# Kernel optimization log

Hardware: AMD Instinct MI355X
Metric: run time of the kernel (lower is better)

Reference implementation:

```python
import jax, jax.numpy as jnp
import numpy as np


def setup_inputs() -> dict:
    key = jax.random.key(0)
    ks = jax.random.split(key, 5)
    B, T, I, H = 32, 2048, 512, 512
    scale = 1.0 / np.sqrt(H)
    return {
        "x": jax.random.normal(ks[0], (B, T, I), dtype=jnp.float32),
        "h_0": jnp.zeros((B, H), dtype=jnp.float32),
        "Wx": jax.random.normal(ks[1], (H, I), dtype=jnp.float32) * scale,
        "bx": jax.random.normal(ks[2], (H,), dtype=jnp.float32) * scale,
        "Wh": jax.random.normal(ks[3], (H, H), dtype=jnp.float32) * scale,
        "bh": jax.random.normal(ks[4], (H,), dtype=jnp.float32) * scale,
    }


def reference(x, h_0, Wx, bx, Wh, bh):
    # Precompute input projection for all timesteps in one big GEMM: [B,T,H]
    x_proj = jnp.einsum("bti,hi->bth", x, Wx) + bx + bh

    def step(h, xp_t):  # h: [B,H], xp_t: [B,H]
        h_new = jnp.tanh(xp_t + h @ Wh.T)
        return h_new, h_new

    # scan over time axis: move T to leading dim
    h_last, outs = jax.lax.scan(step, h_0, jnp.swapaxes(x_proj, 0, 1))
    outputs = jnp.swapaxes(outs, 0, 1)  # [B,T,H]
    return outputs, h_last
```

## Files before the change

### kernel.cpp

```cpp
#include <hip/hip_runtime.h>


constexpr int Bb = 32, Tt = 2048, Ii = 512, Hh = 512;
constexpr int NP = 8;
constexpr int RP = Hh / NP;

static __device__ __forceinline__ float fast_tanh(float x) {
    float ax = fabsf(x);
    float e = __expf(-2.0f * ax);
    float r = (1.0f - e) / (1.0f + e);
    return copysignf(r, x);
}

__global__ __launch_bounds__(256, 2)
void xproj_gemm(const float* __restrict__ x, const float* __restrict__ Wx,
                const float* __restrict__ bx, const float* __restrict__ bh,
                float* __restrict__ xp)
{
    constexpr int BM = 128, BK = 16, LDT = BM + 4;
    __shared__ float As[BK][LDT];
    __shared__ float Bs[BK][LDT];

    const int tid = threadIdx.x;
    const int m0 = blockIdx.x * BM;
    const int n0 = blockIdx.y * BM;
    const int lrow = tid >> 1;
    const int lkh  = (tid & 1) * 8;
    const int tx = tid & 15, ty = tid >> 4;

    float acc[2][2][4][4] = {};

    for (int k0 = 0; k0 < Ii; k0 += BK) {
        float4 a0 = *reinterpret_cast<const float4*>(&x[(size_t)(m0 + lrow) * Ii + k0 + lkh]);
        float4 a1 = *reinterpret_cast<const float4*>(&x[(size_t)(m0 + lrow) * Ii + k0 + lkh + 4]);
        float4 b0 = *reinterpret_cast<const float4*>(&Wx[(size_t)(n0 + lrow) * Ii + k0 + lkh]);
        float4 b1 = *reinterpret_cast<const float4*>(&Wx[(size_t)(n0 + lrow) * Ii + k0 + lkh + 4]);
        __syncthreads();
        As[lkh + 0][lrow] = a0.x; As[lkh + 1][lrow] = a0.y;
        As[lkh + 2][lrow] = a0.z; As[lkh + 3][lrow] = a0.w;
        As[lkh + 4][lrow] = a1.x; As[lkh + 5][lrow] = a1.y;
        As[lkh + 6][lrow] = a1.z; As[lkh + 7][lrow] = a1.w;
        Bs[lkh + 0][lrow] = b0.x; Bs[lkh + 1][lrow] = b0.y;
        Bs[lkh + 2][lrow] = b0.z; Bs[lkh + 3][lrow] = b0.w;
        Bs[lkh + 4][lrow] = b1.x; Bs[lkh + 5][lrow] = b1.y;
        Bs[lkh + 6][lrow] = b1.z; Bs[lkh + 7][lrow] = b1.w;
        __syncthreads();
        #pragma unroll
        for (int k = 0; k < BK; ++k) {
            float4 av[2], bv[2];
            av[0] = *reinterpret_cast<const float4*>(&As[k][ty * 4]);
            av[1] = *reinterpret_cast<const float4*>(&As[k][64 + ty * 4]);
            bv[0] = *reinterpret_cast<const float4*>(&Bs[k][tx * 4]);
            bv[1] = *reinterpret_cast<const float4*>(&Bs[k][64 + tx * 4]);
            #pragma unroll
            for (int rh = 0; rh < 2; ++rh) {
                const float* ap = reinterpret_cast<const float*>(&av[rh]);
                #pragma unroll
                for (int ch = 0; ch < 2; ++ch) {
                    const float* bp = reinterpret_cast<const float*>(&bv[ch]);
                    #pragma unroll
                    for (int i = 0; i < 4; ++i)
                        #pragma unroll
                        for (int j = 0; j < 4; ++j)
                            acc[rh][ch][i][j] += ap[i] * bp[j];
                }
            }
        }
    }

    float4 bias[2];
    #pragma unroll
    for (int ch = 0; ch < 2; ++ch) {
        int cb = n0 + ch * 64 + tx * 4;
        bias[ch] = make_float4(bx[cb] + bh[cb], bx[cb + 1] + bh[cb + 1],
                               bx[cb + 2] + bh[cb + 2], bx[cb + 3] + bh[cb + 3]);
    }
    #pragma unroll
    for (int rh = 0; rh < 2; ++rh)
        #pragma unroll
        for (int i = 0; i < 4; ++i) {
            size_t row = (size_t)(m0 + rh * 64 + ty * 4 + i);
            #pragma unroll
            for (int ch = 0; ch < 2; ++ch) {
                const float* bp = reinterpret_cast<const float*>(&bias[ch]);
                float4 v = make_float4(acc[rh][ch][i][0] + bp[0], acc[rh][ch][i][1] + bp[1],
                                       acc[rh][ch][i][2] + bp[2], acc[rh][ch][i][3] + bp[3]);
                *reinterpret_cast<float4*>(&xp[row * Hh + n0 + ch * 64 + tx * 4]) = v;
            }
        }
}

__global__ void zero_xbuf(unsigned long long* __restrict__ xb)
{
    xb[(size_t)blockIdx.x * 512 + threadIdx.x] = 0ull;
}

__global__ __launch_bounds__(512, 1)
void rnn_scan_mb(const float* __restrict__ Wh, const float* __restrict__ h0,
                 float* __restrict__ out, unsigned long long* __restrict__ xbuf)
{
    const int bid = blockIdx.x;
    const int c = bid & 31;
    const int P = bid >> 5;
    const int tid = threadIdx.x;
    const int w = tid >> 6;
    const int lane = tid & 63;
    const int hf = lane >> 5, lp = lane & 31;
    const int lrow0 = w * 8 + hf * 4;

    __shared__ __align__(16) float hs[Hh];
    __shared__ __align__(16) float pacc[RP][36];

    float4 wreg[4][4];
    #pragma unroll
    for (int s = 0; s < 4; ++s)
        #pragma unroll
        for (int q = 0; q < 4; ++q) {
            const float* ap = &Wh[(size_t)(P * RP + lrow0 + s) * Hh + q * 128 + lp * 4];
            asm volatile("global_load_dwordx4 %0, %1, off"
                         : "=v"(wreg[s][q]) : "v"(ap));
        }
    asm volatile("s_waitcnt vmcnt(0)" ::: "memory");

    hs[tid] = h0[(size_t)c * Hh + tid];

    float* ob = out + (size_t)c * Tt * Hh;
    unsigned long long* xb = xbuf + (size_t)c * 2 * Hh;

    float xp_cur = 0.f;
    if (w == P) xp_cur = ob[P * RP + lane];
    __syncthreads();

    for (int t = 0; t < Tt; ++t) {
        float4 hv[4];
        #pragma unroll
        for (int q = 0; q < 4; ++q)
            hv[q] = *reinterpret_cast<const float4*>(&hs[q * 128 + lp * 4]);
        #pragma unroll
        for (int s = 0; s < 4; ++s) {
            float sum = 0.f;
            #pragma unroll
            for (int q = 0; q < 4; ++q) {
                const float* wq = reinterpret_cast<const float*>(&wreg[s][q]);
                const float* hq = reinterpret_cast<const float*>(&hv[q]);
                sum += wq[0] * hq[0]; sum += wq[1] * hq[1];
                sum += wq[2] * hq[2]; sum += wq[3] * hq[3];
            }
            pacc[lrow0 + s][lp] = sum;
        }
        __syncthreads();

        if (w == P) {
            float ssum = xp_cur;
            #pragma unroll
            for (int q = 0; q < 8; ++q) {
                float4 p4 = *reinterpret_cast<const float4*>(&pacc[lane][q * 4]);
                ssum += (p4.x + p4.y) + (p4.z + p4.w);
            }
            float hval = fast_tanh(ssum);
            ob[(size_t)t * Hh + P * RP + lane] = hval;
            if (t + 1 < Tt) {
                unsigned long long msg =
                    ((unsigned long long)(unsigned)(t + 1) << 32) |
                    (unsigned long long)__float_as_uint(hval);
                __hip_atomic_store(&xb[(size_t)(t & 1) * Hh + P * RP + lane], msg,
                                   __ATOMIC_RELAXED, __HIP_MEMORY_SCOPE_AGENT);
                hs[P * RP + lane] = hval;
                xp_cur = ob[(size_t)(t + 1) * Hh + P * RP + lane];
            } else {
                out[(size_t)Bb * Tt * Hh + (size_t)c * Hh + P * RP + lane] = hval;
            }
        } else if (t + 1 < Tt) {
            const unsigned want = (unsigned)(t + 1);
            unsigned long long msg;
            do {
                msg = __hip_atomic_load(&xb[(size_t)(t & 1) * Hh + w * RP + lane],
                                        __ATOMIC_RELAXED, __HIP_MEMORY_SCOPE_AGENT);
            } while ((unsigned)(msg >> 32) != want);
            hs[w * RP + lane] = __uint_as_float((unsigned)msg);
        }
        __syncthreads();
    }
}

__global__ __launch_bounds__(512)
void rnn_scan_sb(const float* __restrict__ W, const float* __restrict__ h0,
                 float* __restrict__ out)
{
    const int b = blockIdx.x;
    const int j = threadIdx.x;
    __shared__ float hsb[2][Hh];
    hsb[0][j] = h0[(size_t)b * Hh + j];
    __syncthreads();

    float* ob = out + (size_t)b * Tt * Hh;
    const float* wbase = W + (size_t)j * Hh;

    float xp_cur = ob[j];
    int cur = 0;
    for (int t = 0; t < Tt; ++t) {
        float xp_next = (t + 1 < Tt) ? ob[(size_t)(t + 1) * Hh + j] : 0.0f;
        float4 a = make_float4(xp_cur, 0.0f, 0.0f, 0.0f);
        const float* h = hsb[cur];
        #pragma unroll 8
        for (int c4 = 0; c4 < Hh / 4; ++c4) {
            float4 wv = *reinterpret_cast<const float4*>(&wbase[c4 * 4]);
            float4 hv = *reinterpret_cast<const float4*>(&h[c4 * 4]);
            a.x += wv.x * hv.x; a.y += wv.y * hv.y;
            a.z += wv.z * hv.z; a.w += wv.w * hv.w;
        }
        float hn = tanhf((a.x + a.y) + (a.z + a.w));
        hsb[cur ^ 1][j] = hn;
        ob[(size_t)t * Hh + j] = hn;
        xp_cur = xp_next;
        cur ^= 1;
        __syncthreads();
    }
    out[(size_t)Bb * Tt * Hh + (size_t)b * Hh + j] = hsb[cur][j];
}

extern "C" void kernel_launch(void* const* d_in, const int* in_sizes, int n_in,
                              void* d_out, int out_size, void* d_ws, size_t ws_size,
                              hipStream_t stream)
{
    const float* x  = (const float*)d_in[0];
    const float* h0 = (const float*)d_in[1];
    const float* Wx = (const float*)d_in[2];
    const float* bx = (const float*)d_in[3];
    const float* Wh = (const float*)d_in[4];
    const float* bh = (const float*)d_in[5];
    float* out = (float*)d_out;

    dim3 g1(Bb * Tt / 128, Hh / 128);
    xproj_gemm<<<g1, 256, 0, stream>>>(x, Wx, bx, bh, out);

    const size_t xb_bytes = (size_t)Bb * 2 * Hh * sizeof(unsigned long long);
    if (ws_size >= xb_bytes) {
        unsigned long long* xbuf = (unsigned long long*)d_ws;
        zero_xbuf<<<64, 512, 0, stream>>>(xbuf);
        void* args[] = {(void*)&Wh, (void*)&h0, (void*)&out, (void*)&xbuf};
        hipLaunchCooperativeKernel((void*)rnn_scan_mb, dim3(NP * Bb), dim3(512),
                                   args, 0, stream);
    } else {
        rnn_scan_sb<<<Bb, Hh, 0, stream>>>(Wh, h0, out);
    }
}
```

Measured before the change: 3.012 ms.

## Detect same-XCD block groups and poll via L2 with cache-control hints

Each block records its XCC id through s_getreg. After a grid sync, each batch group checks whether all of its blocks share one XCD. If they do, the spin-wait polls with sc0 loads that can hit the shared L2, and it falls back to sc0 sc1 system-coherent loads otherwise. The producer now publishes with an sc1 store before writing the output, and the next xp value is prefetched at the top of each step. This targets the latency of the per-timestep cross-block handshake, at the cost of depending on undocumented cache-coherence behaviour and on how the hardware places blocks.

```diff
diff --git a/kernel.cpp b/kernel.cpp
--- a/kernel.cpp
+++ b/kernel.cpp
@@ -1,4 +1,5 @@
 #include <hip/hip_runtime.h>
+#include <hip/hip_cooperative_groups.h>
 
 
 constexpr int Bb = 32, Tt = 2048, Ii = 512, Hh = 512;
@@ -97,7 +98,8 @@
 
 __global__ __launch_bounds__(512, 1)
 void rnn_scan_mb(const float* __restrict__ Wh, const float* __restrict__ h0,
-                 float* __restrict__ out, unsigned long long* __restrict__ xbuf)
+                 float* __restrict__ out, unsigned long long* __restrict__ xbuf,
+                 unsigned int* __restrict__ xcc_arr)
 {
     const int bid = blockIdx.x;
     const int c = bid & 31;
@@ -110,6 +112,13 @@
 
     __shared__ __align__(16) float hs[Hh];
     __shared__ __align__(16) float pacc[RP][36];
+    __shared__ unsigned int same_sh;
+
+    unsigned int myxcc;
+    asm volatile("s_getreg_b32 %0, hwreg(20, 0, 32)" : "=s"(myxcc));
+    if (tid == 0)
+        __hip_atomic_store(&xcc_arr[bid], myxcc, __ATOMIC_RELAXED,
+                           __HIP_MEMORY_SCOPE_AGENT);
 
     float4 wreg[4][4];
     #pragma unroll
@@ -129,9 +138,22 @@
 
     float xp_cur = 0.f;
     if (w == P) xp_cur = ob[P * RP + lane];
+
+    cooperative_groups::this_grid().sync();
+    if (tid == 0) {
+        unsigned int s = 1;
+        for (int p = 0; p < NP; ++p)
+            s &= (__hip_atomic_load(&xcc_arr[(p << 5) | c], __ATOMIC_RELAXED,
+                                    __HIP_MEMORY_SCOPE_AGENT) == myxcc) ? 1u : 0u;
+        same_sh = s;
+    }
     __syncthreads();
+    const bool samexcd = (same_sh != 0);
 
     for (int t = 0; t < Tt; ++t) {
+        float xp_nxt = 0.f;
+        if (w == P && t + 1 < Tt) xp_nxt = ob[(size_t)(t + 1) * Hh + P * RP + lane];
+
         float4 hv[4];
         #pragma unroll
         for (int q = 0; q < 4; ++q)
@@ -158,25 +180,41 @@
                 ssum += (p4.x + p4.y) + (p4.z + p4.w);
             }
             float hval = fast_tanh(ssum);
-            ob[(size_t)t * Hh + P * RP + lane] = hval;
             if (t + 1 < Tt) {
                 unsigned long long msg =
                     ((unsigned long long)(unsigned)(t + 1) << 32) |
                     (unsigned long long)__float_as_uint(hval);
-                __hip_atomic_store(&xb[(size_t)(t & 1) * Hh + P * RP + lane], msg,
-                                   __ATOMIC_RELAXED, __HIP_MEMORY_SCOPE_AGENT);
+                unsigned long long* pa = &xb[(size_t)(t & 1) * Hh + P * RP + lane];
+                asm volatile("global_store_dwordx2 %0, %1, off sc1"
+                             :: "v"(pa), "v"(msg) : "memory");
+                ob[(size_t)t * Hh + P * RP + lane] = hval;
                 hs[P * RP + lane] = hval;
-                xp_cur = ob[(size_t)(t + 1) * Hh + P * RP + lane];
+                xp_cur = xp_nxt;
             } else {
+                ob[(size_t)t * Hh + P * RP + lane] = hval;
                 out[(size_t)Bb * Tt * Hh + (size_t)c * Hh + P * RP + lane] = hval;
             }
         } else if (t + 1 < Tt) {
-            const unsigned want = (unsigned)(t + 1);
+            const unsigned int want = (unsigned)(t + 1);
+            const unsigned long long* pa = &xb[(size_t)(t & 1) * Hh + w * RP + lane];
             unsigned long long msg;
-            do {
-                msg = __hip_atomic_load(&xb[(size_t)(t & 1) * Hh + w * RP + lane],
-                                        __ATOMIC_RELAXED, __HIP_MEMORY_SCOPE_AGENT);
-            } while ((unsigned)(msg >> 32) != want);
+            bool got = false;
+            while (!got) {
+                if (samexcd) {
+                    #pragma unroll 1
+                    for (int it = 0; it < 8; ++it) {
+                        asm volatile("global_load_dwordx2 %0, %1, off sc0\n\t"
+                                     "s_waitcnt vmcnt(0)"
+                                     : "=v"(msg) : "v"(pa) : "memory");
+                        if ((unsigned)(msg >> 32) == want) { got = true; break; }
+                    }
+                    if (got) break;
+                }
+                asm volatile("global_load_dwordx2 %0, %1, off sc0 sc1\n\t"
+                             "s_waitcnt vmcnt(0)"
+                             : "=v"(msg) : "v"(pa) : "memory");
+                got = ((unsigned)(msg >> 32) == want);
+            }
             hs[w * RP + lane] = __uint_as_float((unsigned)msg);
         }
         __syncthreads();
@@ -234,11 +272,13 @@
     dim3 g1(Bb * Tt / 128, Hh / 128);
     xproj_gemm<<<g1, 256, 0, stream>>>(x, Wx, bx, bh, out);
 
-    const size_t xb_bytes = (size_t)Bb * 2 * Hh * sizeof(unsigned long long);
-    if (ws_size >= xb_bytes) {
+    const size_t xb_bytes  = (size_t)Bb * 2 * Hh * sizeof(unsigned long long);
+    const size_t xcc_bytes = 256 * sizeof(unsigned int);
+    if (ws_size >= xb_bytes + xcc_bytes) {
         unsigned long long* xbuf = (unsigned long long*)d_ws;
+        unsigned int* xcc_arr = (unsigned int*)((char*)d_ws + xb_bytes);
         zero_xbuf<<<64, 512, 0, stream>>>(xbuf);
-        void* args[] = {(void*)&Wh, (void*)&h0, (void*)&out, (void*)&xbuf};
+        void* args[] = {(void*)&Wh, (void*)&h0, (void*)&out, (void*)&xbuf, (void*)&xcc_arr};
         hipLaunchCooperativeKernel((void*)rnn_scan_mb, dim3(NP * Bb), dim3(512),
                                    args, 0, stream);
     } else {
```

Measured after the change: 4.214 ms. 39.9% more time.

## Replace LDS partial-sum reduction with wave shuffles and pipeline cross-block polling

Applied to the files above, without the earlier changes.

The per-step matvec now sums partial dot products with wave-level xor shuffles instead of writing them to a shared pacc array. This removes one __syncthreads per timestep and spreads the tanh/publish work across four lanes in every wave rather than one wave. The hidden state is double-buffered in shared memory, and the next step's x-projection is prefetched before the matvec. Remote-state polling now keeps three inline-asm cache-bypassing loads in flight to cut the latency of each poll. The inline-asm loads have no explicit s_waitcnt before their results are read, which is a correctness and ordering risk.

```diff
diff --git a/kernel.cpp b/kernel.cpp
--- a/kernel.cpp
+++ b/kernel.cpp
@@ -108,8 +108,7 @@
     const int hf = lane >> 5, lp = lane & 31;
     const int lrow0 = w * 8 + hf * 4;
 
-    __shared__ __align__(16) float hs[Hh];
-    __shared__ __align__(16) float pacc[RP][36];
+    __shared__ __align__(16) float hsd[2][Hh];
 
     float4 wreg[4][4];
     #pragma unroll
@@ -122,62 +121,96 @@
         }
     asm volatile("s_waitcnt vmcnt(0)" ::: "memory");
 
-    hs[tid] = h0[(size_t)c * Hh + tid];
+    hsd[0][tid] = h0[(size_t)c * Hh + tid];
 
     float* ob = out + (size_t)c * Tt * Hh;
     unsigned long long* xb = xbuf + (size_t)c * 2 * Hh;
 
+    const bool isPub = (lp < 4);
+    const int grow = P * RP + lrow0 + lp;
+
     float xp_cur = 0.f;
-    if (w == P) xp_cur = ob[P * RP + lane];
+    if (isPub) xp_cur = ob[grow];
     __syncthreads();
 
     for (int t = 0; t < Tt; ++t) {
+        const int cur = t & 1, nxt = cur ^ 1;
+
+        float xp_nxt = 0.f;
+        if (isPub && t + 1 < Tt) xp_nxt = ob[(size_t)(t + 1) * Hh + grow];
+
+        const float* h = hsd[cur];
         float4 hv[4];
         #pragma unroll
         for (int q = 0; q < 4; ++q)
-            hv[q] = *reinterpret_cast<const float4*>(&hs[q * 128 + lp * 4]);
-        #pragma unroll
-        for (int s = 0; s < 4; ++s) {
-            float sum = 0.f;
+            hv[q] = *reinterpret_cast<const float4*>(&h[q * 128 + lp * 4]);
+        float acc0 = 0.f, acc1 = 0.f, acc2 = 0.f, acc3 = 0.f;
+        #pragma unroll
+        for (int q = 0; q < 4; ++q) {
+            const float* hq = reinterpret_cast<const float*>(&hv[q]);
+            const float* w0 = reinterpret_cast<const float*>(&wreg[0][q]);
+            const float* w1 = reinterpret_cast<const float*>(&wreg[1][q]);
+            const float* w2 = reinterpret_cast<const float*>(&wreg[2][q]);
+            const float* w3 = reinterpret_cast<const float*>(&wreg[3][q]);
             #pragma unroll
-            for (int q = 0; q < 4; ++q) {
-                const float* wq = reinterpret_cast<const float*>(&wreg[s][q]);
-                const float* hq = reinterpret_cast<const float*>(&hv[q]);
-                sum += wq[0] * hq[0]; sum += wq[1] * hq[1];
-                sum += wq[2] * hq[2]; sum += wq[3] * hq[3];
-            }
-            pacc[lrow0 + s][lp] = sum;
-        }
-        __syncthreads();
-
-        if (w == P) {
-            float ssum = xp_cur;
-            #pragma unroll
-            for (int q = 0; q < 8; ++q) {
-                float4 p4 = *reinterpret_cast<const float4*>(&pacc[lane][q * 4]);
-                ssum += (p4.x + p4.y) + (p4.z + p4.w);
-            }
-            float hval = fast_tanh(ssum);
-            ob[(size_t)t * Hh + P * RP + lane] = hval;
+            for (int i = 0; i < 4; ++i) {
+                acc0 += w0[i] * hq[i];
+                acc1 += w1[i] * hq[i];
+                acc2 += w2[i] * hq[i];
+                acc3 += w3[i] * hq[i];
+            }
+        }
+
+        #pragma unroll
+        for (int m = 1; m <= 16; m <<= 1) {
+            acc0 += __shfl_xor(acc0, m, 64);
+            acc1 += __shfl_xor(acc1, m, 64);
+            acc2 += __shfl_xor(acc2, m, 64);
+            acc3 += __shfl_xor(acc3, m, 64);
+        }
+
+        if (isPub) {
+            float myacc = (lp == 0) ? acc0 : (lp == 1) ? acc1
+                        : (lp == 2) ? acc2 : acc3;
+            float hval = fast_tanh(xp_cur + myacc);
             if (t + 1 < Tt) {
                 unsigned long long msg =
                     ((unsigned long long)(unsigned)(t + 1) << 32) |
                     (unsigned long long)__float_as_uint(hval);
-                __hip_atomic_store(&xb[(size_t)(t & 1) * Hh + P * RP + lane], msg,
+                __hip_atomic_store(&xb[(size_t)cur * Hh + grow], msg,
                                    __ATOMIC_RELAXED, __HIP_MEMORY_SCOPE_AGENT);
-                hs[P * RP + lane] = hval;
-                xp_cur = ob[(size_t)(t + 1) * Hh + P * RP + lane];
+                ob[(size_t)t * Hh + grow] = hval;
+                hsd[nxt][grow] = hval;
+                xp_cur = xp_nxt;
             } else {
-                out[(size_t)Bb * Tt * Hh + (size_t)c * Hh + P * RP + lane] = hval;
-            }
-        } else if (t + 1 < Tt) {
+                ob[(size_t)t * Hh + grow] = hval;
+                out[(size_t)Bb * Tt * Hh + (size_t)c * Hh + grow] = hval;
+            }
+        }
+
+        if (w != P && t + 1 < Tt) {
             const unsigned want = (unsigned)(t + 1);
-            unsigned long long msg;
-            do {
-                msg = __hip_atomic_load(&xb[(size_t)(t & 1) * Hh + w * RP + lane],
-                                        __ATOMIC_RELAXED, __HIP_MEMORY_SCOPE_AGENT);
-            } while ((unsigned)(msg >> 32) != want);
-            hs[w * RP + lane] = __uint_as_float((unsigned)msg);
+            const unsigned long long* pa = &xb[(size_t)cur * Hh + w * RP + lane];
+            uint2 mA, mB, mC;
+            asm volatile("global_load_dwordx2 %0, %1, off sc0 sc1"
+                         : "=v"(mA) : "v"(pa));
+            asm volatile("global_load_dwordx2 %0, %1, off sc0 sc1"
+                         : "=v"(mB) : "v"(pa));
+            asm volatile("global_load_dwordx2 %0, %1, off sc0 sc1"
+                         : "=v"(mC) : "v"(pa));
+            unsigned val;
+            for (;;) {
+                if (mA.y == want) { val = mA.x; break; }
+                asm volatile("global_load_dwordx2 %0, %1, off sc0 sc1"
+                             : "=v"(mA) : "v"(pa));
+                if (mB.y == want) { val = mB.x; break; }
+                asm volatile("global_load_dwordx2 %0, %1, off sc0 sc1"
+                             : "=v"(mB) : "v"(pa));
+                if (mC.y == want) { val = mC.x; break; }
+                asm volatile("global_load_dwordx2 %0, %1, off sc0 sc1"
+                             : "=v"(mC) : "v"(pa));
+            }
+            hsd[nxt][w * RP + lane] = __uint_as_float(val);
         }
         __syncthreads();
     }
```

Measured after the change: 6.697 ms. +122.3%, slower.

## Restructure multi-block RNN scan to wave-local h slices and one barrier per step

Applied to the files above, without the earlier changes.

Each wave now owns one 64-element slice of h, keeps it in a register, and computes partial dot products for all 64 owned rows over that slice. Partial sums go to a double-buffered shared array, so each timestep needs only one __syncthreads instead of two. The output store is moved after the atomic publish so other blocks see the next h sooner. The catch is that waves read only their own scratch row after an lgkmcnt wait with no barrier, which relies on wave-level LDS ordering, and the reduction shrinks to eight partials per row.

```diff
diff --git a/kernel.cpp b/kernel.cpp
--- a/kernel.cpp
+++ b/kernel.cpp
@@ -105,81 +105,77 @@
     const int tid = threadIdx.x;
     const int w = tid >> 6;
     const int lane = tid & 63;
-    const int hf = lane >> 5, lp = lane & 31;
-    const int lrow0 = w * 8 + hf * 4;
-
-    __shared__ __align__(16) float hs[Hh];
-    __shared__ __align__(16) float pacc[RP][36];
-
-    float4 wreg[4][4];
+
+    __shared__ float hscratch[NP][68];
+    __shared__ float pacc[2][NP][68];
+
+    float4 wreg[16];
     #pragma unroll
-    for (int s = 0; s < 4; ++s)
-        #pragma unroll
-        for (int q = 0; q < 4; ++q) {
-            const float* ap = &Wh[(size_t)(P * RP + lrow0 + s) * Hh + q * 128 + lp * 4];
-            asm volatile("global_load_dwordx4 %0, %1, off"
-                         : "=v"(wreg[s][q]) : "v"(ap));
-        }
+    for (int k = 0; k < 16; ++k) {
+        const float* ap = &Wh[(size_t)(P * RP + lane) * Hh + w * 64 + 4 * k];
+        asm volatile("global_load_dwordx4 %0, %1, off"
+                     : "=v"(wreg[k]) : "v"(ap));
+    }
     asm volatile("s_waitcnt vmcnt(0)" ::: "memory");
-
-    hs[tid] = h0[(size_t)c * Hh + tid];
 
     float* ob = out + (size_t)c * Tt * Hh;
     unsigned long long* xb = xbuf + (size_t)c * 2 * Hh;
 
-    float xp_cur = 0.f;
-    if (w == P) xp_cur = ob[P * RP + lane];
-    __syncthreads();
+    float hcur = h0[(size_t)c * Hh + w * 64 + lane];
+    float xp_cur = (w == P) ? ob[P * RP + lane] : 0.f;
 
     for (int t = 0; t < Tt; ++t) {
-        float4 hv[4];
+        const int d = t & 1;
+
+        hscratch[w][lane] = hcur;
+        asm volatile("s_waitcnt lgkmcnt(0)" ::: "memory");
+
+        float a0 = 0.f, a1 = 0.f, a2 = 0.f, a3 = 0.f;
         #pragma unroll
-        for (int q = 0; q < 4; ++q)
-            hv[q] = *reinterpret_cast<const float4*>(&hs[q * 128 + lp * 4]);
-        #pragma unroll
-        for (int s = 0; s < 4; ++s) {
-            float sum = 0.f;
+        for (int k = 0; k < 16; k += 4) {
+            float4 h0v = *reinterpret_cast<const float4*>(&hscratch[w][4 * k]);
+            float4 h1v = *reinterpret_cast<const float4*>(&hscratch[w][4 * k + 4]);
+            float4 h2v = *reinterpret_cast<const float4*>(&hscratch[w][4 * k + 8]);
+            float4 h3v = *reinterpret_cast<const float4*>(&hscratch[w][4 * k + 12]);
+            const float* w0 = reinterpret_cast<const float*>(&wreg[k]);
+            const float* w1 = reinterpret_cast<const float*>(&wreg[k + 1]);
+            const float* w2 = reinterpret_cast<const float*>(&wreg[k + 2]);
+            const float* w3 = reinterpret_cast<const float*>(&wreg[k + 3]);
+            a0 += w0[0] * h0v.x; a0 += w0[1] * h0v.y; a0 += w0[2] * h0v.z; a0 += w0[3] * h0v.w;
+            a1 += w1[0] * h1v.x; a1 += w1[1] * h1v.y; a1 += w1[2] * h1v.z; a1 += w1[3] * h1v.w;
+            a2 += w2[0] * h2v.x; a2 += w2[1] * h2v.y; a2 += w2[2] * h2v.z; a2 += w2[3] * h2v.w;
+            a3 += w3[0] * h3v.x; a3 += w3[1] * h3v.y; a3 += w3[2] * h3v.z; a3 += w3[3] * h3v.w;
+        }
+        pacc[d][w][lane] = (a0 + a1) + (a2 + a3);
+        __syncthreads();
+
+        if (w == P) {
+            float s = xp_cur;
             #pragma unroll
-            for (int q = 0; q < 4; ++q) {
-                const float* wq = reinterpret_cast<const float*>(&wreg[s][q]);
-                const float* hq = reinterpret_cast<const float*>(&hv[q]);
-                sum += wq[0] * hq[0]; sum += wq[1] * hq[1];
-                sum += wq[2] * hq[2]; sum += wq[3] * hq[3];
-            }
-            pacc[lrow0 + s][lp] = sum;
-        }
-        __syncthreads();
-
-        if (w == P) {
-            float ssum = xp_cur;
-            #pragma unroll
-            for (int q = 0; q < 8; ++q) {
-                float4 p4 = *reinterpret_cast<const float4*>(&pacc[lane][q * 4]);
-                ssum += (p4.x + p4.y) + (p4.z + p4.w);
-            }
-            float hval = fast_tanh(ssum);
-            ob[(size_t)t * Hh + P * RP + lane] = hval;
+            for (int g = 0; g < NP; ++g) s += pacc[d][g][lane];
+            float hval = fast_tanh(s);
+            hcur = hval;
             if (t + 1 < Tt) {
                 unsigned long long msg =
                     ((unsigned long long)(unsigned)(t + 1) << 32) |
                     (unsigned long long)__float_as_uint(hval);
-                __hip_atomic_store(&xb[(size_t)(t & 1) * Hh + P * RP + lane], msg,
+                __hip_atomic_store(&xb[(size_t)d * Hh + P * RP + lane], msg,
                                    __ATOMIC_RELAXED, __HIP_MEMORY_SCOPE_AGENT);
-                hs[P * RP + lane] = hval;
+                ob[(size_t)t * Hh + P * RP + lane] = hval;
                 xp_cur = ob[(size_t)(t + 1) * Hh + P * RP + lane];
             } else {
+                ob[(size_t)t * Hh + P * RP + lane] = hval;
                 out[(size_t)Bb * Tt * Hh + (size_t)c * Hh + P * RP + lane] = hval;
             }
         } else if (t + 1 < Tt) {
             const unsigned want = (unsigned)(t + 1);
             unsigned long long msg;
             do {
-                msg = __hip_atomic_load(&xb[(size_t)(t & 1) * Hh + w * RP + lane],
+                msg = __hip_atomic_load(&xb[(size_t)d * Hh + w * RP + lane],
                                         __ATOMIC_RELAXED, __HIP_MEMORY_SCOPE_AGENT);
             } while ((unsigned)(msg >> 32) != want);
-            hs[w * RP + lane] = __uint_as_float((unsigned)msg);
-        }
-        __syncthreads();
+            hcur = __uint_as_float((unsigned)msg);
+        }
     }
 }
 
```

Result: slower. 3.298 ms (+9.5%).
